# Kernel optimization log

Measured on AMD Instinct MI355X. Metric: run time of the kernel, lower is better.

## Reference

```python
import jax, jax.numpy as jnp
import numpy as np

N, K, D = 262144, 256, 128
SCALE = 0.1
LOG2PI = float(np.log(2.0 * np.pi))


def setup_inputs() -> dict:
    key = jax.random.key(0)
    k_in, k_mu, k_ls, k_noise = jax.random.split(key, 4)
    return {
        "input": jax.random.normal(k_in, (N, D), dtype=jnp.float32),
        "means": jax.random.normal(k_mu, (K, D), dtype=jnp.float32),
        "log_stds": jax.random.normal(k_ls, (K, D), dtype=jnp.float32) * 0.5,
        "weights": jnp.ones((K,), dtype=jnp.float32),
        "noise": jax.random.normal(k_noise, (N, D), dtype=jnp.float32),
    }


def _gmm_forward(x, means, log_stds, weights, noise):
    d = x.shape[-1]
    # Diagonal-Gaussian log-prob per component, via GEMM decomposition:
    inv_var = jnp.exp(-2.0 * log_stds)                      # [K, D]
    quad = (
        (x * x) @ inv_var.T                                  # [N, K]
        - 2.0 * (x @ (means * inv_var).T)                    # [N, K]
        + jnp.sum(means * means * inv_var, axis=-1)          # [K]
    )
    log_p_x_z = -0.5 * (quad + d * LOG2PI) - jnp.sum(log_stds, axis=-1)  # [N, K]
    log_p_z = jax.nn.log_softmax(weights)                    # [K]
    joint = log_p_x_z + log_p_z                              # [N, K]
    p_z_x = jax.nn.softmax(joint + 1e-8, axis=-1)            # [N, K]
    idxs = jnp.argmax(p_z_x, axis=-1)                        # [N]
    Q = jnp.mean(jax.lax.stop_gradient(p_z_x) * joint)       # scalar
    # Resample from the selected component (noise replaces randn_like)
    resampled_x = means[idxs] + jnp.exp(log_stds[idxs]) * noise * SCALE
    return resampled_x, idxs, Q


def reference(input, means, log_stds, weights, noise):
    return _gmm_forward(input, means, log_stds, weights, noise)
```

## Files before the change

kernel.cpp:

```cpp
#include <hip/hip_runtime.h>
#include <math.h>

#define N_ROWS 262144
#define K_COMP 256
#define D_DIM  128
#define BN 32
#define KIN 256

typedef _Float16 half8v __attribute__((ext_vector_type(8)));
typedef _Float16 half4v __attribute__((ext_vector_type(4)));
typedef float    f32x4  __attribute__((ext_vector_type(4)));

static __device__ __constant__ float kLOG2PI = 1.8378770664093453f;

__global__ __launch_bounds__(128) void gmm_prep(
    const float* __restrict__ means, const float* __restrict__ log_stds,
    const float* __restrict__ weights,
    _Float16* __restrict__ Bhi, _Float16* __restrict__ Blo,
    float* __restrict__ sigma, float* __restrict__ ck, double* __restrict__ wsq)
{
    int k = blockIdx.x;
    int d = threadIdx.x;
    float ls = log_stds[k * D_DIM + d];
    float mu = means[k * D_DIM + d];
    float iv = expf(-2.0f * ls);
    float m2 = -2.0f * mu * iv;
    sigma[k * D_DIM + d] = expf(ls);

    {
        int c = k >> 4;
        #pragma unroll
        for (int t = 0; t < 2; ++t) {
            int kin = t * 128 + d;
            float val = t ? m2 : iv;
            int s = kin >> 5;
            int l = ((kin >> 3) & 3) * 16 + (k & 15);
            int j = kin & 7;
            int lin = ((c * 8 + s) * 64 + l) * 8 + j;
            _Float16 hi = (_Float16)val;
            Bhi[lin] = hi;
            Blo[lin] = (_Float16)(val - (float)hi);
        }
    }

    float c = mu * mu * iv;
    float s = ls;
    float w1 = weights[d], w2 = weights[d + 128];
    float wm = fmaxf(w1, w2);

    __shared__ float red[8];
    int lane = d & 63, wv = d >> 6;
    #pragma unroll
    for (int o = 32; o > 0; o >>= 1) {
        c += __shfl_down(c, o, 64);
        s += __shfl_down(s, o, 64);
        wm = fmaxf(wm, __shfl_down(wm, o, 64));
    }
    if (lane == 0) { red[wv] = c; red[2 + wv] = s; red[4 + wv] = wm; }
    __syncthreads();
    float csum = red[0] + red[1];
    float ssum = red[2] + red[3];
    float wmax = fmaxf(red[4], red[5]);
    float we = expf(w1 - wmax) + expf(w2 - wmax);
    #pragma unroll
    for (int o = 32; o > 0; o >>= 1) we += __shfl_down(we, o, 64);
    if (lane == 0) red[6 + wv] = we;
    __syncthreads();
    if (d == 0) {
        float wsum = red[6] + red[7];
        float lw = weights[k] - (wmax + logf(wsum));
        ck[k] = -0.5f * (csum + (float)D_DIM * kLOG2PI) - ssum + lw;
        if (k == 0) *wsq = 0.0;
    }
}

__global__ __launch_bounds__(256, 4) void gmm_main(
    const float* __restrict__ x, const float* __restrict__ noise,
    const float* __restrict__ means, const float* __restrict__ sigma,
    const _Float16* __restrict__ Bhi, const _Float16* __restrict__ Blo,
    const float* __restrict__ ck,
    float* __restrict__ out_x, float* __restrict__ out_idx, double* __restrict__ wsq)
{
    __shared__ char  sA[2][BN * 256];
    __shared__ float sCk[K_COMP];
    __shared__ float sMax[BN][4];
    __shared__ int   sAm [BN][4];
    __shared__ float sEs [BN][4];
    __shared__ float sQs [BN][4];
    __shared__ int   sIdx[BN];

    const int tid = threadIdx.x;
    const int w   = tid >> 6;
    const int l   = tid & 63;
    const int lm  = l & 15;
    const int lh  = l >> 4;
    const long n0 = (long)blockIdx.x * BN;

    sCk[tid] = ck[tid];

    const float4* xg = (const float4*)(x + (size_t)n0 * D_DIM);

    #pragma unroll
    for (int it = 0; it < 4; ++it) {
        int g = it * 256 + tid;
        int row = g >> 5, d4 = g & 31;
        float4 xv = xg[g];
        float xe[4] = {xv.x, xv.y, xv.z, xv.w};
        half4v h, lo;
        #pragma unroll
        for (int cc = 0; cc < 4; ++cc) {
            float vv = xe[cc] * xe[cc];
            _Float16 a = (_Float16)vv;
            h[cc] = a; lo[cc] = (_Float16)(vv - (float)a);
        }
        unsigned off = ((unsigned)(row * 256 + d4 * 8)) ^ ((unsigned)(row & 7) << 4);
        *(half4v*)(sA[0] + off) = h;
        *(half4v*)(sA[1] + off) = lo;
    }
    __syncthreads();

    f32x4 acc[2][4];
    #pragma unroll
    for (int rf = 0; rf < 2; ++rf)
        #pragma unroll
        for (int cf = 0; cf < 4; ++cf)
            acc[rf][cf] = (f32x4){0.0f, 0.0f, 0.0f, 0.0f};

    const half8v* Bh = (const half8v*)Bhi;
    const half8v* Bl = (const half8v*)Blo;

    #pragma unroll 2
    for (int s = 0; s < 4; ++s) {
        half8v ah[2], al[2], bh4[4], bl4[4];
        #pragma unroll
        for (int rf = 0; rf < 2; ++rf) {
            int row = rf * 16 + lm;
            unsigned off = ((unsigned)(row * 256 + s * 64 + lh * 16))
                         ^ ((unsigned)(row & 7) << 4);
            ah[rf] = *(const half8v*)(sA[0] + off);
            al[rf] = *(const half8v*)(sA[1] + off);
        }
        #pragma unroll
        for (int cf = 0; cf < 4; ++cf) {
            int bidx = ((w * 4 + cf) * 8 + s) * 64 + l;
            bh4[cf] = Bh[bidx];
            bl4[cf] = Bl[bidx];
        }
        #pragma unroll
        for (int rf = 0; rf < 2; ++rf)
            #pragma unroll
            for (int cf = 0; cf < 4; ++cf) {
                acc[rf][cf] = __builtin_amdgcn_mfma_f32_16x16x32_f16(ah[rf], bh4[cf], acc[rf][cf], 0, 0, 0);
                acc[rf][cf] = __builtin_amdgcn_mfma_f32_16x16x32_f16(ah[rf], bl4[cf], acc[rf][cf], 0, 0, 0);
                acc[rf][cf] = __builtin_amdgcn_mfma_f32_16x16x32_f16(al[rf], bh4[cf], acc[rf][cf], 0, 0, 0);
            }
    }

    float4 xv2[4];
    #pragma unroll
    for (int it = 0; it < 4; ++it) xv2[it] = xg[it * 256 + tid];

    __syncthreads();

    #pragma unroll
    for (int it = 0; it < 4; ++it) {
        int g = it * 256 + tid;
        int row = g >> 5, d4 = g & 31;
        float xe[4] = {xv2[it].x, xv2[it].y, xv2[it].z, xv2[it].w};
        half4v h, lo;
        #pragma unroll
        for (int cc = 0; cc < 4; ++cc) {
            float v = xe[cc];
            _Float16 a = (_Float16)v;
            h[cc] = a; lo[cc] = (_Float16)(v - (float)a);
        }
        unsigned off = ((unsigned)(row * 256 + d4 * 8)) ^ ((unsigned)(row & 7) << 4);
        *(half4v*)(sA[0] + off) = h;
        *(half4v*)(sA[1] + off) = lo;
    }
    __syncthreads();

    #pragma unroll 2
    for (int s = 4; s < 8; ++s) {
        half8v ah[2], al[2], bh4[4], bl4[4];
        #pragma unroll
        for (int rf = 0; rf < 2; ++rf) {
            int row = rf * 16 + lm;
            unsigned off = ((unsigned)(row * 256 + (s - 4) * 64 + lh * 16))
                         ^ ((unsigned)(row & 7) << 4);
            ah[rf] = *(const half8v*)(sA[0] + off);
            al[rf] = *(const half8v*)(sA[1] + off);
        }
        #pragma unroll
        for (int cf = 0; cf < 4; ++cf) {
            int bidx = ((w * 4 + cf) * 8 + s) * 64 + l;
            bh4[cf] = Bh[bidx];
            bl4[cf] = Bl[bidx];
        }
        #pragma unroll
        for (int rf = 0; rf < 2; ++rf)
            #pragma unroll
            for (int cf = 0; cf < 4; ++cf) {
                acc[rf][cf] = __builtin_amdgcn_mfma_f32_16x16x32_f16(ah[rf], bh4[cf], acc[rf][cf], 0, 0, 0);
                acc[rf][cf] = __builtin_amdgcn_mfma_f32_16x16x32_f16(ah[rf], bl4[cf], acc[rf][cf], 0, 0, 0);
                acc[rf][cf] = __builtin_amdgcn_mfma_f32_16x16x32_f16(al[rf], bh4[cf], acc[rf][cf], 0, 0, 0);
            }
    }

    float ckv[4];
    #pragma unroll
    for (int cf = 0; cf < 4; ++cf) ckv[cf] = sCk[w * 64 + cf * 16 + lm];

    #pragma unroll
    for (int rf = 0; rf < 2; ++rf) {
        #pragma unroll
        for (int reg = 0; reg < 4; ++reg) {
            int row = rf * 16 + lh * 4 + reg;
            float jv[4];
            float m = -INFINITY; int am = 0;
            #pragma unroll
            for (int cf = 0; cf < 4; ++cf) {
                float v = fmaf(-0.5f, acc[rf][cf][reg], ckv[cf]);
                jv[cf] = v;
                int col = w * 64 + cf * 16 + lm;
                if (v > m) { m = v; am = col; }
            }
            #pragma unroll
            for (int o = 1; o < 16; o <<= 1) {
                float om = __shfl_xor(m, o, 16);
                int   oa = __shfl_xor(am, o, 16);
                if (om > m || (om == m && oa < am)) { m = om; am = oa; }
            }
            float es = 0.0f, qs = 0.0f;
            #pragma unroll
            for (int cf = 0; cf < 4; ++cf) {
                float e = __expf(jv[cf] - m);
                es += e; qs = fmaf(e, jv[cf], qs);
            }
            #pragma unroll
            for (int o = 1; o < 16; o <<= 1) {
                es += __shfl_xor(es, o, 16);
                qs += __shfl_xor(qs, o, 16);
            }
            if (lm == 0) {
                sMax[row][w] = m; sAm[row][w] = am;
                sEs [row][w] = es; sQs[row][w] = qs;
            }
        }
    }

    const int wv = tid >> 6, lane = tid & 63;
    float2 nvv[8];
    #pragma unroll
    for (int r8 = 0; r8 < 8; ++r8)
        nvv[r8] = *(const float2*)&noise[(n0 + wv * 8 + r8) * D_DIM + lane * 2];

    __syncthreads();

    float qv = 0.0f;
    if (tid < BN) {
        const int row = tid;
        float m = sMax[row][0]; int am = sAm[row][0];
        float es = sEs[row][0], qs = sQs[row][0];
        #pragma unroll
        for (int w2 = 1; w2 < 4; ++w2) {
            float mw = sMax[row][w2];
            if (mw > m) {
                float f = __expf(m - mw);
                es = es * f + sEs[row][w2];
                qs = qs * f + sQs[row][w2];
                m = mw; am = sAm[row][w2];
            } else {
                float f = __expf(mw - m);
                es += sEs[row][w2] * f;
                qs += sQs[row][w2] * f;
            }
        }
        sIdx[row] = am;
        float q = __fdividef(qs, es);
        #pragma unroll
        for (int o = 1; o < 64; o <<= 1) q += __shfl_xor(q, o, 64);
        qv = q;
    }
    __syncthreads();

    #pragma unroll
    for (int r8 = 0; r8 < 8; ++r8) {
        const int row = wv * 8 + r8;
        const int idx = sIdx[row];
        const long n = n0 + row;
        float2 mv = *(const float2*)&means[idx * D_DIM + lane * 2];
        float2 sv = *(const float2*)&sigma[idx * D_DIM + lane * 2];
        float2 ov;
        ov.x = mv.x + sv.x * nvv[r8].x * 0.1f;
        ov.y = mv.y + sv.y * nvv[r8].y * 0.1f;
        *(float2*)&out_x[n * D_DIM + lane * 2] = ov;
    }
    if (tid < BN) out_idx[n0 + tid] = (float)sIdx[tid];

    if (tid == 0) atomicAdd(wsq, (double)qv);
}

__global__ void gmm_finalize(const double* __restrict__ wsq, float* __restrict__ out_q)
{
    *out_q = (float)(*wsq * (1.0 / ((double)N_ROWS * (double)K_COMP)));
}

extern "C" void kernel_launch(void* const* d_in, const int* in_sizes, int n_in,
                              void* d_out, int out_size, void* d_ws, size_t ws_size,
                              hipStream_t stream)
{
    const float* x        = (const float*)d_in[0];
    const float* means    = (const float*)d_in[1];
    const float* log_stds = (const float*)d_in[2];
    const float* weights  = (const float*)d_in[3];
    const float* noise    = (const float*)d_in[4];

    float* out_x   = (float*)d_out;
    float* out_idx = (float*)d_out + (size_t)N_ROWS * D_DIM;
    float* out_q   = out_idx + N_ROWS;

    float*     ws    = (float*)d_ws;
    _Float16*  Bhi   = (_Float16*)ws;
    _Float16*  Blo   = (_Float16*)(ws + 32768);
    float*     sigma = ws + 65536;
    float*     ckp   = ws + 98304;
    double*    wsq   = (double*)(ws + 98560);

    hipLaunchKernelGGL(gmm_prep, dim3(K_COMP), dim3(D_DIM), 0, stream,
                       means, log_stds, weights, Bhi, Blo, sigma, ckp, wsq);
    hipLaunchKernelGGL(gmm_main, dim3(N_ROWS / BN), dim3(256), 0, stream,
                       x, noise, means, sigma, Bhi, Blo, ckp, out_x, out_idx, wsq);
    hipLaunchKernelGGL(gmm_finalize, dim3(1), dim3(1), 0, stream, wsq, out_q);
}
```

Baseline: 412.8 us.

## Interleave hi/lo B fragments and fold finalize into main kernel via ticket

The hi and lo fp16 halves of the B operand now sit side by side in one buffer, so each lane fetches them from adjacent 16-byte chunks instead of two separate arrays. The separate single-thread finalize launch is dropped: the last block to finish, found through an atomic ticket counter, writes the scaled Q. This removes one kernel launch and may improve B-load locality, at the cost of a threadfence and an extra atomic per block.

```diff
diff --git a/kernel.cpp b/kernel.cpp
--- a/kernel.cpp
+++ b/kernel.cpp
@@ -16,8 +16,9 @@
 __global__ __launch_bounds__(128) void gmm_prep(
     const float* __restrict__ means, const float* __restrict__ log_stds,
     const float* __restrict__ weights,
-    _Float16* __restrict__ Bhi, _Float16* __restrict__ Blo,
-    float* __restrict__ sigma, float* __restrict__ ck, double* __restrict__ wsq)
+    _Float16* __restrict__ Bil,
+    float* __restrict__ sigma, float* __restrict__ ck, double* __restrict__ wsq,
+    int* __restrict__ cnt)
 {
     int k = blockIdx.x;
     int d = threadIdx.x;
@@ -36,10 +37,10 @@
             int s = kin >> 5;
             int l = ((kin >> 3) & 3) * 16 + (k & 15);
             int j = kin & 7;
-            int lin = ((c * 8 + s) * 64 + l) * 8 + j;
+            size_t base = ((size_t)((c * 8 + s) * 64 + l)) * 16 + j;
             _Float16 hi = (_Float16)val;
-            Bhi[lin] = hi;
-            Blo[lin] = (_Float16)(val - (float)hi);
+            Bil[base]     = hi;
+            Bil[base + 8] = (_Float16)(val - (float)hi);
         }
     }
 
@@ -70,16 +71,17 @@
         float wsum = red[6] + red[7];
         float lw = weights[k] - (wmax + logf(wsum));
         ck[k] = -0.5f * (csum + (float)D_DIM * kLOG2PI) - ssum + lw;
-        if (k == 0) *wsq = 0.0;
+        if (k == 0) { *wsq = 0.0; *cnt = 0; }
     }
 }
 
 __global__ __launch_bounds__(256, 4) void gmm_main(
     const float* __restrict__ x, const float* __restrict__ noise,
     const float* __restrict__ means, const float* __restrict__ sigma,
-    const _Float16* __restrict__ Bhi, const _Float16* __restrict__ Blo,
+    const _Float16* __restrict__ Bil,
     const float* __restrict__ ck,
-    float* __restrict__ out_x, float* __restrict__ out_idx, double* __restrict__ wsq)
+    float* __restrict__ out_x, float* __restrict__ out_idx, float* __restrict__ out_q,
+    double* __restrict__ wsq, int* __restrict__ cnt)
 {
     __shared__ char  sA[2][BN * 256];
     __shared__ float sCk[K_COMP];
@@ -126,8 +128,7 @@
         for (int cf = 0; cf < 4; ++cf)
             acc[rf][cf] = (f32x4){0.0f, 0.0f, 0.0f, 0.0f};
 
-    const half8v* Bh = (const half8v*)Bhi;
-    const half8v* Bl = (const half8v*)Blo;
+    const half8v* Bi = (const half8v*)Bil;
 
     #pragma unroll 2
     for (int s = 0; s < 4; ++s) {
@@ -142,9 +143,9 @@
         }
         #pragma unroll
         for (int cf = 0; cf < 4; ++cf) {
-            int bidx = ((w * 4 + cf) * 8 + s) * 64 + l;
-            bh4[cf] = Bh[bidx];
-            bl4[cf] = Bl[bidx];
+            int p = (((w * 4 + cf) * 8 + s) * 64 + l) * 2;
+            bh4[cf] = Bi[p];
+            bl4[cf] = Bi[p + 1];
         }
         #pragma unroll
         for (int rf = 0; rf < 2; ++rf)
@@ -193,9 +194,9 @@
         }
         #pragma unroll
         for (int cf = 0; cf < 4; ++cf) {
-            int bidx = ((w * 4 + cf) * 8 + s) * 64 + l;
-            bh4[cf] = Bh[bidx];
-            bl4[cf] = Bl[bidx];
+            int p = (((w * 4 + cf) * 8 + s) * 64 + l) * 2;
+            bh4[cf] = Bi[p];
+            bl4[cf] = Bi[p + 1];
         }
         #pragma unroll
         for (int rf = 0; rf < 2; ++rf)
@@ -298,12 +299,15 @@
     }
     if (tid < BN) out_idx[n0 + tid] = (float)sIdx[tid];
 
-    if (tid == 0) atomicAdd(wsq, (double)qv);
-}
-
-__global__ void gmm_finalize(const double* __restrict__ wsq, float* __restrict__ out_q)
-{
-    *out_q = (float)(*wsq * (1.0 / ((double)N_ROWS * (double)K_COMP)));
+    if (tid == 0) {
+        atomicAdd(wsq, (double)qv);
+        __threadfence();
+        int ticket = atomicAdd(cnt, 1);
+        if (ticket == (int)gridDim.x - 1) {
+            double tot = atomicAdd(wsq, 0.0);
+            *out_q = (float)(tot * (1.0 / ((double)N_ROWS * (double)K_COMP)));
+        }
+    }
 }
 
 extern "C" void kernel_launch(void* const* d_in, const int* in_sizes, int n_in,
@@ -321,15 +325,14 @@
     float* out_q   = out_idx + N_ROWS;
 
     float*     ws    = (float*)d_ws;
-    _Float16*  Bhi   = (_Float16*)ws;
-    _Float16*  Blo   = (_Float16*)(ws + 32768);
+    _Float16*  Bil   = (_Float16*)ws;
     float*     sigma = ws + 65536;
     float*     ckp   = ws + 98304;
     double*    wsq   = (double*)(ws + 98560);
+    int*       cnt   = (int*)(ws + 98562);
 
     hipLaunchKernelGGL(gmm_prep, dim3(K_COMP), dim3(D_DIM), 0, stream,
-                       means, log_stds, weights, Bhi, Blo, sigma, ckp, wsq);
+                       means, log_stds, weights, Bil, sigma, ckp, wsq, cnt);
     hipLaunchKernelGGL(gmm_main, dim3(N_ROWS / BN), dim3(256), 0, stream,
-                       x, noise, means, sigma, Bhi, Blo, ckp, out_x, out_idx, wsq);
-    hipLaunchKernelGGL(gmm_finalize, dim3(1), dim3(1), 0, stream, wsq, out_q);
+                       x, noise, means, sigma, Bil, ckp, out_x, out_idx, out_q, wsq, cnt);
 }
```

New measurement: 819.5 us. 1.98x slower.
